# Optimization experiments

Measured on AMD Instinct MI355X. Metric: run time of the kernel, lower is better.

Reference implementation:

```python
import jax, jax.numpy as jnp
import numpy as np


def setup_inputs() -> dict:
    key = jax.random.key(0)
    ks = jax.random.split(key, 8)
    b, n, K, d, MC = 32, 64, 512, 256, 2
    # soft codebook assignments per slot (bounded convex weights)
    encodings = jax.nn.softmax(jax.random.normal(ks[0], (b, n, K), jnp.float32), axis=-1)
    # hypersphere-initialized means (unit-norm rows)
    mu = jax.random.normal(ks[1], (K, d), jnp.float32)
    mu_embeddings = mu / jnp.linalg.norm(mu, axis=-1, keepdims=True)
    sigma_embeddings = jax.random.uniform(ks[2], (K, d), jnp.float32)
    fc1_w = jax.random.normal(ks[3], (K, d, d), jnp.float32) * (1.0 / np.sqrt(d))
    fc1_b = jax.random.normal(ks[4], (K, d), jnp.float32) * 0.02
    fc2_w = jax.random.normal(ks[5], (K, d, d), jnp.float32) * (1.0 / np.sqrt(d))
    fc2_b = jax.random.normal(ks[6], (K, d), jnp.float32) * 0.02
    eps = jax.random.normal(ks[7], (b, MC, n, d), jnp.float32)  # reparam noise
    return {"encodings": encodings, "mu_embeddings": mu_embeddings,
            "sigma_embeddings": sigma_embeddings, "fc1_w": fc1_w, "fc1_b": fc1_b,
            "fc2_w": fc2_w, "fc2_b": fc2_b, "eps": eps}


def reference(encodings, mu_embeddings, sigma_embeddings, fc1_w, fc1_b, fc2_w, fc2_b, eps):
    b, n, K = encodings.shape
    m = eps.shape[1]
    # per-slot Gaussian params from codebook mixture
    slot_mu = jnp.einsum('bnk,kd->bnd', encodings, mu_embeddings)          # (b,n,d)
    slot_sigma = jnp.exp(0.5 * jnp.einsum('bnk,kd->bnd', encodings, sigma_embeddings))
    # reparameterized MC samples: (b,m,n,d)
    slots = slot_mu[:, None] + slot_sigma[:, None] * eps
    # per-token dynamic 2-layer MLP weights (mixture over codebook)
    fc1w = jnp.einsum('bnk,kgh->bngh', encodings, fc1_w)  # (b,n,d,d)
    fc1b = jnp.einsum('bnk,kg->bng', encodings, fc1_b)    # (b,n,d)
    fc2w = jnp.einsum('bnk,kgh->bngh', encodings, fc2_w)
    fc2b = jnp.einsum('bnk,kg->bng', encodings, fc2_b)
    slots = jax.nn.relu(jnp.einsum('bmng,bngh->bmnh', slots, fc1w) + fc1b[:, None])
    slots = jax.nn.relu(jnp.einsum('bmng,bngh->bmnh', slots, fc2w) + fc2b[:, None])
    # rearrange 'b m n d -> (b m) n d'
    return slots.reshape(b * m, n, slots.shape[-1])
```

## Files before the change

kernel.cpp:

```cpp
#include <hip/hip_runtime.h>
#include <hip/hip_bf16.h>

typedef unsigned short u16;
typedef __attribute__((ext_vector_type(8))) short shortx8;
typedef __attribute__((ext_vector_type(4))) float floatx4;

__device__ __forceinline__ float bf2f(u16 u) {
    union { unsigned int ui; float f; } x; x.ui = ((unsigned int)u) << 16; return x.f;
}
__device__ __forceinline__ u16 f2b(float f) {
    union { float f; unsigned int u; } x; x.f = f;
    unsigned int r = (x.u + 0x7fffu + ((x.u >> 16) & 1u)) >> 16;
    return (u16)r;
}
__device__ __forceinline__ void glds16(const void* g, void* l) {
    __builtin_amdgcn_global_load_lds((const __attribute__((address_space(1))) void*)g,
                                     (__attribute__((address_space(3))) void*)l, 16, 0, 0);
}

__global__ __launch_bounds__(256) void cvt_bf16_kernel(const float* __restrict__ src,
                                                       u16* __restrict__ dst, int n) {
    int i = (blockIdx.x * 256 + threadIdx.x) * 4;
    if (i + 3 < n) {
        float4 v = *(const float4*)&src[i];
        ushort4 o; o.x = f2b(v.x); o.y = f2b(v.y); o.z = f2b(v.z); o.w = f2b(v.w);
        *(ushort4*)&dst[i] = o;
    }
}

__global__ __launch_bounds__(256) void build_bsmall_t(const float* __restrict__ mu,
                                                      const float* __restrict__ sg,
                                                      const float* __restrict__ b1,
                                                      const float* __restrict__ b2,
                                                      u16* __restrict__ Bs) {
    __shared__ float t[32][33];
    const float* src;
    int z = blockIdx.z;
    if (z == 0) src = mu; else if (z == 1) src = sg; else if (z == 2) src = b1; else src = b2;
    int k0 = blockIdx.x * 32, c0 = blockIdx.y * 32;
    int r = threadIdx.x >> 3, c4 = (threadIdx.x & 7) * 4;
    float4 v = *(const float4*)&src[(size_t)(k0 + r) * 256 + c0 + c4];
    t[r][c4] = v.x; t[r][c4 + 1] = v.y; t[r][c4 + 2] = v.z; t[r][c4 + 3] = v.w;
    __syncthreads();
    ushort4 o;
    o.x = f2b(t[c4 + 0][r]); o.y = f2b(t[c4 + 1][r]);
    o.z = f2b(t[c4 + 2][r]); o.w = f2b(t[c4 + 3][r]);
    *(ushort4*)&Bs[(size_t)(z * 256 + c0 + r) * 512 + k0 + c4] = o;
}

__global__ __launch_bounds__(256) void cvt_transpose(const float* __restrict__ W,
                                                     u16* __restrict__ Bt) {
    __shared__ float t[64][33];
    int n0 = blockIdx.x * 32, k0 = blockIdx.y * 64;
    int r = threadIdx.x >> 2;
    int c = (threadIdx.x & 3) * 8;
    float4 v0 = *(const float4*)&W[(size_t)(k0 + r) * 65536 + n0 + c];
    float4 v1 = *(const float4*)&W[(size_t)(k0 + r) * 65536 + n0 + c + 4];
    t[r][c + 0] = v0.x; t[r][c + 1] = v0.y; t[r][c + 2] = v0.z; t[r][c + 3] = v0.w;
    t[r][c + 4] = v1.x; t[r][c + 5] = v1.y; t[r][c + 6] = v1.z; t[r][c + 7] = v1.w;
    __syncthreads();
    int nr = threadIdx.x >> 3;
    int kk = (threadIdx.x & 7) * 8;
    shortx8 o;
    #pragma unroll
    for (int i = 0; i < 8; i++) o[i] = (short)f2b(t[kk + i][nr]);
    *(shortx8*)&Bt[(size_t)(n0 + nr) * 512 + k0 + kk] = o;
}

__global__ __launch_bounds__(256) void slots_kernel(const float* __restrict__ P,
                                                    const float* __restrict__ eps,
                                                    float* __restrict__ slots) {
    int t = blockIdx.x, d = threadIdx.x;
    float mu = P[(size_t)t * 1024 + d];
    float sg = expf(0.5f * P[(size_t)t * 1024 + 256 + d]);
    int b = t >> 6, n = t & 63;
    #pragma unroll
    for (int m = 0; m < 2; m++) {
        float e = eps[(size_t)(((b * 2 + m) * 64) + n) * 256 + d];
        slots[(size_t)t * 512 + m * 256 + d] = mu + sg * e;
    }
}

__global__ __launch_bounds__(256, 2) void gemm_small(const u16* __restrict__ A,
                                                     const u16* __restrict__ B,
                                                     float* __restrict__ C,
                                                     int N, int K,
                                                     int nbx_l2, int bypx_l2) {
    __shared__ __align__(16) u16 As[128 * 64];
    __shared__ __align__(16) u16 Bs[128 * 64];
    int tid = threadIdx.x;
    int wave = tid >> 6, lane = tid & 63;

    int id = blockIdx.x;
    int xcd = id & 7, sq = id >> 3;
    int by = (xcd << bypx_l2) + (sq >> nbx_l2);
    int bx = sq & ((1 << nbx_l2) - 1);
    int m0 = bx * 128, n0 = by * 128;
    int wm = wave >> 1, wn = wave & 1;

    floatx4 acc[4][4];
    #pragma unroll
    for (int r = 0; r < 4; r++)
        #pragma unroll
        for (int c = 0; c < 4; c++)
            #pragma unroll
            for (int q = 0; q < 4; q++) acc[r][c][q] = 0.f;

    int lrsub = lane >> 3, kcl = lane & 7;
    const u16* gA[4]; const u16* gB[4]; u16* lA[4]; u16* lB[4];
    #pragma unroll
    for (int j = 0; j < 4; j++) {
        int r0 = (wave * 4 + j) * 8;
        int row = r0 + lrsub;
        int kof = (kcl ^ (row & 7)) * 8;
        gA[j] = A + (size_t)(m0 + row) * K + kof;
        gB[j] = B + (size_t)(n0 + row) * K + kof;
        lA[j] = As + r0 * 64;
        lB[j] = Bs + r0 * 64;
    }

    int arb = wm * 64 + (lane & 15);
    int brb = wn * 64 + (lane & 15);
    int axr = arb & 7, bxr = brb & 7;
    int cl0 = lane >> 4;

    for (int k0 = 0; k0 < K; k0 += 64) {
        #pragma unroll
        for (int j = 0; j < 4; j++) glds16(gA[j] + k0, lA[j]);
        #pragma unroll
        for (int j = 0; j < 4; j++) glds16(gB[j] + k0, lB[j]);
        __syncthreads();
        #pragma unroll
        for (int s = 0; s < 2; s++) {
            shortx8 af[4], bf[4];
            int ac = ((s * 4 + cl0) ^ axr) * 8;
            int bc = ((s * 4 + cl0) ^ bxr) * 8;
            #pragma unroll
            for (int r = 0; r < 4; r++) af[r] = *(const shortx8*)(As + (arb + r * 16) * 64 + ac);
            #pragma unroll
            for (int c = 0; c < 4; c++) bf[c] = *(const shortx8*)(Bs + (brb + c * 16) * 64 + bc);
            #pragma unroll
            for (int r = 0; r < 4; r++)
                #pragma unroll
                for (int c = 0; c < 4; c++)
                    acc[r][c] = __builtin_amdgcn_mfma_f32_16x16x32_bf16(af[r], bf[c], acc[r][c], 0, 0, 0);
        }
        __syncthreads();
    }

    int crow0 = m0 + wm * 64 + (lane >> 4) * 4;
    int ccol  = n0 + wn * 64 + (lane & 15);
    #pragma unroll
    for (int r = 0; r < 4; r++)
        #pragma unroll
        for (int c = 0; c < 4; c++)
            #pragma unroll
            for (int q = 0; q < 4; q++)
                C[(size_t)(crow0 + r * 16 + q) * N + ccol + c * 16] = acc[r][c][q];
}

__global__ __launch_bounds__(256) void init_y(const float* __restrict__ P,
                                              float* __restrict__ Y, int bias_col) {
    int t = blockIdx.x, h = threadIdx.x;
    float b = P[(size_t)t * 1024 + bias_col + h];
    Y[((size_t)t * 2 + 0) * 256 + h] = b;
    Y[((size_t)t * 2 + 1) * 256 + h] = b;
}

__global__ __launch_bounds__(256, 2) void fused_mlp(const u16* __restrict__ Eb,
                                                    const u16* __restrict__ Bt,
                                                    const float* __restrict__ S,
                                                    float* __restrict__ Y,
                                                    int relu_s) {
    __shared__ __align__(16) u16 As[128 * 64];
    __shared__ __align__(16) u16 Bs[2][64 * 64];
    __shared__ float sl[16 * 2 * 128];
    int tid = threadIdx.x;
    int wave = tid >> 6, lane = tid & 63;

    int id = blockIdx.x;
    int xcd = id & 7;
    int rest = id >> 3;
    int tt = rest & 15;
    int chi = rest >> 4;
    int combo = chi * 8 + xcd;
    int hh = combo >> 3;
    int gg = combo & 7;
    int m0 = tt * 128;
    int h0 = hh * 64;
    int g0 = gg * 32;

    int wm = wave >> 1, wn = wave & 1;
    int lrsub = lane >> 3, kcl = lane & 7;
    int kof = (kcl ^ lrsub) * 8;

    const u16* gAb = Eb + (size_t)(m0 + wave * 32 + lrsub) * 512 + kof;
    const u16* gBb = Bt + ((size_t)g0 * 256 + h0 + wave * 16 + lrsub) * 512 + kof;
    u16* lAb = As + wave * 2048;
    u16* lB0 = &Bs[0][wave * 1024];
    u16* lB1 = &Bs[1][wave * 1024];

    int arb = wm * 64 + (lane & 15);
    int brb = wn * 32 + (lane & 15);
    int axr = arb & 7, bxr = brb & 7;
    int cl0 = lane >> 4;

    floatx4 yreg[2][4][2];
    #pragma unroll
    for (int m = 0; m < 2; m++)
        #pragma unroll
        for (int r = 0; r < 4; r++)
            #pragma unroll
            for (int c = 0; c < 2; c++)
                #pragma unroll
                for (int q = 0; q < 4; q++) yreg[m][r][c][q] = 0.f;

    #pragma unroll 1
    for (int half = 0; half < 2; half++) {
        __syncthreads();
        {
            int g = tid & 15, m = (tid >> 4) & 1, tb = tid >> 5;
            for (int p = 0; p < 16; p++) {
                int t = tb + p * 8;
                float v = S[((size_t)(m0 + t) * 2 + m) * 256 + g0 + half * 16 + g];
                if (relu_s) v = fmaxf(v, 0.f);
                sl[(g * 2 + m) * 128 + t] = v;
            }
        }

        #pragma unroll 1
        for (int gp = 0; gp < 8; gp++) {
            size_t gof0 = (size_t)(half * 16 + 2 * gp) * 131072;
            size_t gof1 = gof0 + 131072;
            floatx4 acc[2][4][2];
            #pragma unroll
            for (int u = 0; u < 2; u++)
                #pragma unroll
                for (int r = 0; r < 4; r++)
                    #pragma unroll
                    for (int c = 0; c < 2; c++)
                        #pragma unroll
                        for (int q = 0; q < 4; q++) acc[u][r][c][q] = 0.f;

            for (int k0 = 0; k0 < 512; k0 += 64) {
                #pragma unroll
                for (int j = 0; j < 4; j++) glds16(gAb + j * 4096 + k0, lAb + j * 512);
                #pragma unroll
                for (int j = 0; j < 2; j++) glds16(gBb + gof0 + j * 4096 + k0, lB0 + j * 512);
                #pragma unroll
                for (int j = 0; j < 2; j++) glds16(gBb + gof1 + j * 4096 + k0, lB1 + j * 512);
                __syncthreads();
                #pragma unroll
                for (int s = 0; s < 2; s++) {
                    shortx8 af[4], bf[2][2];
                    int ac = ((s * 4 + cl0) ^ axr) * 8;
                    int bc = ((s * 4 + cl0) ^ bxr) * 8;
                    #pragma unroll
                    for (int r = 0; r < 4; r++) af[r] = *(const shortx8*)(As + (arb + r * 16) * 64 + ac);
                    #pragma unroll
                    for (int u = 0; u < 2; u++)
                        #pragma unroll
                        for (int c = 0; c < 2; c++)
                            bf[u][c] = *(const shortx8*)(&Bs[u][(brb + c * 16) * 64 + bc]);
                    #pragma unroll
                    for (int r = 0; r < 4; r++)
                        #pragma unroll
                        for (int u = 0; u < 2; u++)
                            #pragma unroll
                            for (int c = 0; c < 2; c++)
                                acc[u][r][c] = __builtin_amdgcn_mfma_f32_16x16x32_bf16(af[r], bf[u][c], acc[u][r][c], 0, 0, 0);
                }
                __syncthreads();
            }

            #pragma unroll
            for (int u = 0; u < 2; u++) {
                int gi = 2 * gp + u;
                #pragma unroll
                for (int m = 0; m < 2; m++) {
                    float4 sq[4];
                    #pragma unroll
                    for (int r = 0; r < 4; r++)
                        sq[r] = *(const float4*)&sl[(gi * 2 + m) * 128 + wm * 64 + cl0 * 4 + r * 16];
                    #pragma unroll
                    for (int r = 0; r < 4; r++)
                        #pragma unroll
                        for (int c = 0; c < 2; c++)
                            #pragma unroll
                            for (int q = 0; q < 4; q++)
                                yreg[m][r][c][q] += ((const float*)&sq[r])[q] * acc[u][r][c][q];
                }
            }
        }
    }

    int l16 = lane & 15;
    #pragma unroll
    for (int m = 0; m < 2; m++)
        #pragma unroll
        for (int r = 0; r < 4; r++)
            #pragma unroll
            for (int c = 0; c < 2; c++)
                #pragma unroll
                for (int q = 0; q < 4; q++) {
                    int t = m0 + wm * 64 + cl0 * 4 + r * 16 + q;
                    int h = h0 + wn * 32 + c * 16 + l16;
                    atomicAdd(&Y[((size_t)t * 2 + m) * 256 + h], yreg[m][r][c][q]);
                }
}

__global__ __launch_bounds__(256) void final_out(const float* __restrict__ Y,
                                                 float* __restrict__ out) {
    int t = blockIdx.x, h = threadIdx.x;
    int b = t >> 6, n = t & 63;
    #pragma unroll
    for (int m = 0; m < 2; m++)
        out[((size_t)((b * 2 + m) * 64) + n) * 256 + h] =
            fmaxf(Y[((size_t)t * 2 + m) * 256 + h], 0.f);
}

extern "C" void kernel_launch(void* const* d_in, const int* in_sizes, int n_in,
                              void* d_out, int out_size, void* d_ws, size_t ws_size,
                              hipStream_t stream) {
    const float* enc = (const float*)d_in[0];
    const float* mu  = (const float*)d_in[1];
    const float* sg  = (const float*)d_in[2];
    const float* f1w = (const float*)d_in[3];
    const float* f1b = (const float*)d_in[4];
    const float* f2w = (const float*)d_in[5];
    const float* f2b = (const float*)d_in[6];
    const float* eps = (const float*)d_in[7];
    float* out = (float*)d_out;

    size_t off = 0;
    auto alloc = [&](size_t b) -> char* {
        char* p = (char*)d_ws + off; off += (b + 255) & ~(size_t)255; return p;
    };
    u16*   Eb    = (u16*)  alloc((size_t)2048 * 512 * 2);
    float* P     = (float*)alloc((size_t)2048 * 1024 * 4);
    float* slots = (float*)alloc((size_t)2048 * 512 * 4);
    float* Y1    = (float*)alloc((size_t)2048 * 512 * 4);
    float* Y2    = (float*)alloc((size_t)2048 * 512 * 4);
    u16*   Bsm   = (u16*)  alloc((size_t)1024 * 512 * 2);
    u16*   Bt    = (u16*)  alloc((size_t)65536 * 512 * 2);

    cvt_bf16_kernel<<<1024, 256, 0, stream>>>(enc, Eb, 2048 * 512);
    build_bsmall_t<<<dim3(16, 8, 4), 256, 0, stream>>>(mu, sg, f1b, f2b, Bsm);
    gemm_small<<<128, 256, 0, stream>>>(Eb, Bsm, P, 1024, 512, 4, 0);
    slots_kernel<<<2048, 256, 0, stream>>>(P, eps, slots);

    cvt_transpose<<<dim3(2048, 8), 256, 0, stream>>>(f1w, Bt);
    init_y<<<2048, 256, 0, stream>>>(P, Y1, 512);
    fused_mlp<<<512, 256, 0, stream>>>(Eb, Bt, slots, Y1, 0);

    cvt_transpose<<<dim3(2048, 8), 256, 0, stream>>>(f2w, Bt);
    init_y<<<2048, 256, 0, stream>>>(P, Y2, 768);
    fused_mlp<<<512, 256, 0, stream>>>(Eb, Bt, Y1, Y2, 1);

    final_out<<<2048, 256, 0, stream>>>(Y2, out);
}
```

Before: 637.2 us.

## Double-buffer LDS tiles with async prefetch and read S scales directly

```diff
diff --git a/kernel.cpp b/kernel.cpp
--- a/kernel.cpp
+++ b/kernel.cpp
@@ -172,9 +172,8 @@
                                                     const float* __restrict__ S,
                                                     float* __restrict__ Y,
                                                     int relu_s) {
-    __shared__ __align__(16) u16 As[128 * 64];
-    __shared__ __align__(16) u16 Bs[2][64 * 64];
-    __shared__ float sl[16 * 2 * 128];
+    __shared__ __align__(16) u16 As[2][128 * 64];
+    __shared__ __align__(16) u16 Bs[2][2][64 * 64];
     int tid = threadIdx.x;
     int wave = tid >> 6, lane = tid & 63;
 
@@ -196,9 +195,6 @@
 
     const u16* gAb = Eb + (size_t)(m0 + wave * 32 + lrsub) * 512 + kof;
     const u16* gBb = Bt + ((size_t)g0 * 256 + h0 + wave * 16 + lrsub) * 512 + kof;
-    u16* lAb = As + wave * 2048;
-    u16* lB0 = &Bs[0][wave * 1024];
-    u16* lB1 = &Bs[1][wave * 1024];
 
     int arb = wm * 64 + (lane & 15);
     int brb = wn * 32 + (lane & 15);
@@ -215,84 +211,92 @@
                 #pragma unroll
                 for (int q = 0; q < 4; q++) yreg[m][r][c][q] = 0.f;
 
+    #pragma unroll
+    for (int j = 0; j < 4; j++) glds16(gAb + j * 4096, &As[0][wave * 2048 + j * 512]);
+    #pragma unroll
+    for (int j = 0; j < 2; j++) glds16(gBb + j * 4096, &Bs[0][0][wave * 1024 + j * 512]);
+    #pragma unroll
+    for (int j = 0; j < 2; j++) glds16(gBb + 131072 + j * 4096, &Bs[0][1][wave * 1024 + j * 512]);
+
+    const float* Sb = S + (size_t)(m0 + wm * 64 + cl0 * 4) * 512 + g0;
+
     #pragma unroll 1
-    for (int half = 0; half < 2; half++) {
-        __syncthreads();
-        {
-            int g = tid & 15, m = (tid >> 4) & 1, tb = tid >> 5;
-            for (int p = 0; p < 16; p++) {
-                int t = tb + p * 8;
-                float v = S[((size_t)(m0 + t) * 2 + m) * 256 + g0 + half * 16 + g];
-                if (relu_s) v = fmaxf(v, 0.f);
-                sl[(g * 2 + m) * 128 + t] = v;
+    for (int gp = 0; gp < 16; gp++) {
+        floatx4 acc[2][4][2];
+        #pragma unroll
+        for (int u = 0; u < 2; u++)
+            #pragma unroll
+            for (int r = 0; r < 4; r++)
+                #pragma unroll
+                for (int c = 0; c < 2; c++)
+                    #pragma unroll
+                    for (int q = 0; q < 4; q++) acc[u][r][c][q] = 0.f;
+
+        #pragma unroll
+        for (int ks = 0; ks < 8; ++ks) {
+            const int cb = ks & 1;
+            const int nb = cb ^ 1;
+            {
+                const int nk = ((ks + 1) & 7) * 64;
+                const int ngp = (ks == 7) ? ((gp + 1) & 15) : gp;
+                const size_t ng = (size_t)(2 * ngp) * 131072;
+                #pragma unroll
+                for (int j = 0; j < 4; j++)
+                    glds16(gAb + j * 4096 + nk, &As[nb][wave * 2048 + j * 512]);
+                #pragma unroll
+                for (int j = 0; j < 2; j++)
+                    glds16(gBb + ng + j * 4096 + nk, &Bs[nb][0][wave * 1024 + j * 512]);
+                #pragma unroll
+                for (int j = 0; j < 2; j++)
+                    glds16(gBb + ng + 131072 + j * 4096 + nk, &Bs[nb][1][wave * 1024 + j * 512]);
             }
-        }
-
-        #pragma unroll 1
-        for (int gp = 0; gp < 8; gp++) {
-            size_t gof0 = (size_t)(half * 16 + 2 * gp) * 131072;
-            size_t gof1 = gof0 + 131072;
-            floatx4 acc[2][4][2];
-            #pragma unroll
-            for (int u = 0; u < 2; u++)
+            asm volatile("s_waitcnt vmcnt(8)" ::: "memory");
+            __builtin_amdgcn_s_barrier();
+            __builtin_amdgcn_sched_barrier(0);
+            #pragma unroll
+            for (int s = 0; s < 2; s++) {
+                shortx8 af[4], bf[2][2];
+                int ac = ((s * 4 + cl0) ^ axr) * 8;
+                int bc = ((s * 4 + cl0) ^ bxr) * 8;
                 #pragma unroll
                 for (int r = 0; r < 4; r++)
+                    af[r] = *(const shortx8*)(&As[cb][(arb + r * 16) * 64 + ac]);
+                #pragma unroll
+                for (int u = 0; u < 2; u++)
                     #pragma unroll
                     for (int c = 0; c < 2; c++)
-                        #pragma unroll
-                        for (int q = 0; q < 4; q++) acc[u][r][c][q] = 0.f;
-
-            for (int k0 = 0; k0 < 512; k0 += 64) {
-                #pragma unroll
-                for (int j = 0; j < 4; j++) glds16(gAb + j * 4096 + k0, lAb + j * 512);
-                #pragma unroll
-                for (int j = 0; j < 2; j++) glds16(gBb + gof0 + j * 4096 + k0, lB0 + j * 512);
-                #pragma unroll
-                for (int j = 0; j < 2; j++) glds16(gBb + gof1 + j * 4096 + k0, lB1 + j * 512);
-                __syncthreads();
-                #pragma unroll
-                for (int s = 0; s < 2; s++) {
-                    shortx8 af[4], bf[2][2];
-                    int ac = ((s * 4 + cl0) ^ axr) * 8;
-                    int bc = ((s * 4 + cl0) ^ bxr) * 8;
-                    #pragma unroll
-                    for (int r = 0; r < 4; r++) af[r] = *(const shortx8*)(As + (arb + r * 16) * 64 + ac);
+                        bf[u][c] = *(const shortx8*)(&Bs[cb][u][(brb + c * 16) * 64 + bc]);
+                #pragma unroll
+                for (int r = 0; r < 4; r++)
                     #pragma unroll
                     for (int u = 0; u < 2; u++)
                         #pragma unroll
                         for (int c = 0; c < 2; c++)
-                            bf[u][c] = *(const shortx8*)(&Bs[u][(brb + c * 16) * 64 + bc]);
+                            acc[u][r][c] = __builtin_amdgcn_mfma_f32_16x16x32_bf16(af[r], bf[u][c], acc[u][r][c], 0, 0, 0);
+            }
+            __builtin_amdgcn_sched_barrier(0);
+            __builtin_amdgcn_s_barrier();
+        }
+
+        #pragma unroll
+        for (int u = 0; u < 2; u++) {
+            int gi = 2 * gp + u;
+            #pragma unroll
+            for (int m = 0; m < 2; m++)
+                #pragma unroll
+                for (int r = 0; r < 4; r++)
                     #pragma unroll
-                    for (int r = 0; r < 4; r++)
-                        #pragma unroll
-                        for (int u = 0; u < 2; u++)
-                            #pragma unroll
-                            for (int c = 0; c < 2; c++)
-                                acc[u][r][c] = __builtin_amdgcn_mfma_f32_16x16x32_bf16(af[r], bf[u][c], acc[u][r][c], 0, 0, 0);
-                }
-                __syncthreads();
-            }
-
-            #pragma unroll
-            for (int u = 0; u < 2; u++) {
-                int gi = 2 * gp + u;
-                #pragma unroll
-                for (int m = 0; m < 2; m++) {
-                    float4 sq[4];
-                    #pragma unroll
-                    for (int r = 0; r < 4; r++)
-                        sq[r] = *(const float4*)&sl[(gi * 2 + m) * 128 + wm * 64 + cl0 * 4 + r * 16];
-                    #pragma unroll
-                    for (int r = 0; r < 4; r++)
+                    for (int q = 0; q < 4; q++) {
+                        float sv = Sb[(size_t)(r * 16 + q) * 512 + m * 256 + gi];
+                        if (relu_s) sv = fmaxf(sv, 0.f);
                         #pragma unroll
                         for (int c = 0; c < 2; c++)
-                            #pragma unroll
-                            for (int q = 0; q < 4; q++)
-                                yreg[m][r][c][q] += ((const float*)&sq[r])[q] * acc[u][r][c][q];
-                }
-            }
+                            yreg[m][r][c][q] += sv * acc[u][r][c][q];
+                    }
         }
     }
+
+    asm volatile("s_waitcnt vmcnt(0)" ::: "memory");
 
     int l16 = lane & 15;
     #pragma unroll
```

Result: slower. 707.2 us (+11.0%).
